# Optimization experiments

Measured on AMD Instinct MI355X. Metric: run time of the kernel, lower is better.

The kernel has to match this reference:

```python
import jax, jax.numpy as jnp
import numpy as np

SLOPE = 0.01   # LeakyReLU default negative slope
EPS = 1e-5     # InstanceNorm eps
PAD = 6        # shift-search border

def _pad(x):
    # ReplicationPad (1,1) on H and W (depth pad is 0, depth==1 anyway)
    return jnp.pad(x, ((0, 0), (0, 0), (1, 1), (1, 1)), mode='edge')

def _conv(x, w, b):
    y = jax.lax.conv_general_dilated(x, w, (1, 1), 'VALID',
                                     dimension_numbers=('NCHW', 'OIHW', 'NCHW'))
    return y + b[None, :, None, None]

def _inorm(x):
    # InstanceNorm3d (affine=False) over (D,H,W); D==1 so over (H,W) per (b,c)
    m = jnp.mean(x, axis=(-2, -1), keepdims=True)
    v = jnp.mean((x - m) ** 2, axis=(-2, -1), keepdims=True)
    return (x - m) * jax.lax.rsqrt(v + EPS)

def _lrelu(x):
    return jnp.where(x >= 0, x, SLOPE * x)

def setup_inputs() -> dict:
    key = jax.random.key(0)
    ks = jax.random.split(key, 8)
    B, H, W = 8, 256, 256
    xIn = jax.random.normal(ks[0], (B, 1, H, W), jnp.float32)
    target = jax.random.normal(ks[1], (B, 1, H, W), jnp.float32)
    w0 = jax.random.normal(ks[2], (64, 1, 3, 3), jnp.float32) * 0.1
    b0 = jax.random.normal(ks[3], (64,), jnp.float32) * 0.1
    ws = jax.random.normal(ks[4], (7, 64, 64, 3, 3), jnp.float32) * 0.05
    bs = jax.random.normal(ks[5], (7, 64), jnp.float32) * 0.05
    wp = jax.random.normal(ks[6], (1, 64, 3, 3), jnp.float32) * 0.05
    bp = jax.random.normal(ks[7], (1,), jnp.float32) * 0.05
    return {'xIn': xIn, 'target': target, 'w0': w0, 'b0': b0,
            'ws': ws, 'bs': bs, 'wp': wp, 'bp': bp}

def reference(xIn, target, w0, b0, ws, bs, wp, bp):
    x = _lrelu(_inorm(_conv(_pad(xIn), w0, b0)))
    for i in range(7):
        x = _lrelu(_inorm(_conv(_pad(x), ws[i], bs[i])))
    # projection + residual
    hr = _conv(_pad(x), wp, bp) + xIn  # (B,1,H,W)

    # vectorized findBestLoss: 13x13 shift search
    B, C, H, W = hr.shape
    h, w = H - 2 * PAD, W - 2 * PAD
    t = hr.dtype.type(0) + target[..., PAD:H - PAD, PAD:W - PAD]  # (B,C,h,w)
    offs = jnp.stack(jnp.meshgrid(jnp.arange(13), jnp.arange(13),
                                  indexing='ij'), -1).reshape(-1, 2)  # (169,2)

    def _slice(off):
        return jax.lax.dynamic_slice(hr, (0, 0, off[0], off[1]), (B, C, h, w))

    crops = jax.vmap(_slice)(offs)  # (169,B,C,h,w)
    eq = jax.lax.stop_gradient(
        jnp.mean(t[None] - crops, axis=(2, 3, 4), keepdims=True))  # detached equalizer
    losses = jnp.mean((crops + eq - t[None]) ** 2, axis=(2, 3, 4))  # (169,B)
    loss = jnp.mean(jnp.min(losses, axis=0))
    return hr, loss
```

## Files before the change

### kernel.cpp

```cpp
#include <hip/hip_runtime.h>

#define B_ 8
#define C_ 64
#define HW_ 65536
#define SLOPE_ 0.01f
#define EPS_ 1e-5f
#define CROP_ 244
#define NPIX_ 59536.0f

typedef unsigned short u16;
typedef __attribute__((ext_vector_type(8))) _Float16 f16x8;
typedef __attribute__((ext_vector_type(2))) _Float16 f16x2;
typedef __attribute__((ext_vector_type(4))) float f32x4;

__device__ __forceinline__ int clampi(int v, int lo, int hi) { return v < lo ? lo : (v > hi ? hi : v); }

__device__ __forceinline__ u16 f2h(float f) {
    union { _Float16 h; u16 u; } v; v.h = (_Float16)f; return v.u;
}
__device__ __forceinline__ float h2f(u16 b) {
    union { u16 u; _Float16 h; } v; v.u = b; return (float)v.h;
}
__device__ __forceinline__ f16x2 lrelu2(f16x2 a) {
    const f16x2 z = {(_Float16)0.f, (_Float16)0.f};
    const f16x2 sl = {(_Float16)SLOPE_, (_Float16)SLOPE_};
    return __builtin_elementwise_max(a, z) + sl * __builtin_elementwise_min(a, z);
}

__global__ void wtrans_kernel(const float* __restrict__ ws, u16* __restrict__ wH) {
    int idx = blockIdx.x * 256 + threadIdx.x;
    if (idx >= 7 * 36864) return;
    int l = idx / 36864;
    int rem = idx - l * 36864;
    int frag = rem >> 9;
    int lj = rem & 511;
    int lane = lj >> 3, j = lj & 7;
    int tap = frag >> 3, kb = (frag >> 2) & 1, mt = frag & 3;
    int oc = (mt << 4) + (lane & 15);
    int ic = (kb << 5) + ((lane >> 4) << 3) + j;
    wH[idx] = f2h(ws[((l * 64 + oc) * 64 + ic) * 9 + tap]);
}

__global__ __launch_bounds__(256) void conv0_kernel(
    const float* __restrict__ xin, const float* __restrict__ w0,
    const float* __restrict__ b0, u16* __restrict__ yout) {
    __shared__ float w0s[576];
    __shared__ float b0s[64];
    int tid = threadIdx.x;
    for (int i = tid; i < 576; i += 256) w0s[i] = w0[i];
    if (tid < 64) b0s[tid] = b0[tid];
    __syncthreads();
    int b = blockIdx.x & 7;
    int px = (blockIdx.x >> 3) * 256 + tid;
    int pxg = (b << 16) + px;
    int y = px >> 8, x = px & 255;
    float xv[9];
#pragma unroll
    for (int ky = 0; ky < 3; ky++)
#pragma unroll
        for (int kx = 0; kx < 3; kx++)
            xv[ky * 3 + kx] = xin[(b << 16) + (clampi(y + ky - 1, 0, 255) << 8) + clampi(x + kx - 1, 0, 255)];
    float acc[64];
#pragma unroll
    for (int k = 0; k < 64; k++) acc[k] = b0s[k];
#pragma unroll
    for (int t = 0; t < 9; t++) {
        float v = xv[t];
#pragma unroll
        for (int k = 0; k < 64; k++) acc[k] = fmaf(v, w0s[k * 9 + t], acc[k]);
    }
    uint4* op = (uint4*)(yout + ((size_t)pxg << 6));
#pragma unroll
    for (int c8 = 0; c8 < 8; c8++) {
        uint4 o;
        o.x = (unsigned)f2h(acc[c8 * 8 + 0]) | ((unsigned)f2h(acc[c8 * 8 + 1]) << 16);
        o.y = (unsigned)f2h(acc[c8 * 8 + 2]) | ((unsigned)f2h(acc[c8 * 8 + 3]) << 16);
        o.z = (unsigned)f2h(acc[c8 * 8 + 4]) | ((unsigned)f2h(acc[c8 * 8 + 5]) << 16);
        o.w = (unsigned)f2h(acc[c8 * 8 + 6]) | ((unsigned)f2h(acc[c8 * 8 + 7]) << 16);
        op[c8] = o;
    }
}

__global__ __launch_bounds__(256) void stats0_kernel(const u16* __restrict__ yin, float* __restrict__ partial) {
    __shared__ float red[4][64][2];
    int tid = threadIdx.x;
    int b = blockIdx.x & 7, tile = blockIdx.x >> 3;
    int pxl = tid >> 3, c8 = tid & 7;
    float s[8], s2[8];
#pragma unroll
    for (int i = 0; i < 8; i++) { s[i] = 0.f; s2[i] = 0.f; }
    for (int it = 0; it < 8; it++) {
        int px = (tile << 8) + (it << 5) + pxl;
        f16x8 v = *(const f16x8*)(yin + ((((size_t)(b << 16)) + px) << 6) + (c8 << 3));
#pragma unroll
        for (int i = 0; i < 8; i++) {
            float f = (float)v[i];
            s[i] += f; s2[i] += f * f;
        }
    }
#pragma unroll
    for (int msk = 8; msk <= 32; msk <<= 1)
#pragma unroll
        for (int i = 0; i < 8; i++) {
            s[i] += __shfl_xor(s[i], msk);
            s2[i] += __shfl_xor(s2[i], msk);
        }
    int lane = tid & 63, wv = tid >> 6;
    if (lane < 8) {
#pragma unroll
        for (int i = 0; i < 8; i++) {
            red[wv][lane * 8 + i][0] = s[i];
            red[wv][lane * 8 + i][1] = s2[i];
        }
    }
    __syncthreads();
    if (tid < 128) {
        int oc = tid >> 1, k2 = tid & 1;
        float v = red[0][oc][k2] + red[1][oc][k2] + red[2][oc][k2] + red[3][oc][k2];
        partial[(((b << 8) + tile) << 7) + (oc << 1) + k2] = v;
    }
}

__global__ __launch_bounds__(64) void statfin_kernel(const float* __restrict__ partial, float* __restrict__ normp, int ntiles) {
    int b = blockIdx.x >> 6, oc = blockIdx.x & 63;
    int lane = threadIdx.x;
    float s = 0.f, s2 = 0.f;
    for (int t = lane; t < ntiles; t += 64) {
        const float* p = partial + (((size_t)(b * ntiles + t)) << 7) + (oc << 1);
        s += p[0]; s2 += p[1];
    }
#pragma unroll
    for (int msk = 1; msk < 64; msk <<= 1) { s += __shfl_xor(s, msk); s2 += __shfl_xor(s2, msk); }
    if (lane == 0) {
        float mean = s * (1.0f / HW_);
        float var = s2 * (1.0f / HW_) - mean * mean;
        float inv = rsqrtf(var + EPS_);
        normp[blockIdx.x * 2] = inv;
        normp[blockIdx.x * 2 + 1] = -mean * inv;
    }
}

#define CM_CHUNKS 4896
__global__ __launch_bounds__(256, 1) void conv_mid_kernel(
    const u16* __restrict__ yin, const float* __restrict__ normp,
    const u16* __restrict__ wH, const float* __restrict__ bias,
    u16* __restrict__ yout, float* __restrict__ partial) {
    __shared__ u16 s_w[36864];
    __shared__ u16 s_in[612 * 64];
    __shared__ float s_red[4 * 64 * 2];
    __shared__ unsigned s_invk[32];
    __shared__ unsigned s_betak[32];
    __shared__ float s_bias[64];

    int tid = threadIdx.x;
    int bid = blockIdx.x;
    int b = bid & 7;
    int xs = (bid >> 3) & 15;
    int yq = bid >> 7;
    int x0 = xs << 4;

    if (tid < 64) s_bias[tid] = bias[tid];
    if (tid < 32) {
        float4 ld = ((const float4*)(normp + (b << 7)))[tid];
        union { unsigned u; f16x2 h; } iv, bv;
        iv.h = (f16x2){(_Float16)ld.x, (_Float16)ld.z};
        bv.h = (f16x2){(_Float16)ld.y, (_Float16)ld.w};
        s_invk[tid] = iv.u;
        s_betak[tid] = bv.u;
    }
    for (int i = tid; i < 4608; i += 256)
        ((uint4*)s_w)[i] = ((const uint4*)wH)[i];
    __syncthreads();

    {
        int y0 = yq << 7;
        for (int chunk = tid; chunk < CM_CHUNKS; chunk += 256) {
            int px = chunk >> 3, c8 = chunk & 7;
            int row = px / 18;
            int col = px - row * 18;
            int iy = clampi(y0 - 1 + row, 0, 255);
            int ix = clampi(x0 - 1 + col, 0, 255);
            union { uint4 q; f16x2 h2[4]; } ui, uo;
            ui.q = *(const uint4*)(yin + ((((size_t)(b << 16)) + (iy << 8) + ix) << 6) + (c8 << 3));
#pragma unroll
            for (int p = 0; p < 4; p++) {
                union { unsigned u; f16x2 h; } iv, bv;
                iv.u = s_invk[(c8 << 2) + p];
                bv.u = s_betak[(c8 << 2) + p];
                uo.h2[p] = lrelu2(ui.h2[p] * iv.h + bv.h);
            }
            *(uint4*)(&s_in[(px << 6) + ((c8 ^ (px & 7)) << 3)]) = uo.q;
        }
    }
    __syncthreads();

    int lane = tid & 63, wv = tid >> 6;
    int m = lane & 15, q = lane >> 4;
    int r0 = wv << 3;

    for (int r = 0; r < 4; r++) {
        int y0 = ((yq << 2) + r) << 5;
        uint4 pf[20];
        if (r < 3) {
            int y0n = y0 + 32;
#pragma unroll
            for (int k = 0; k < 20; k++) {
                int chunk = tid + (k << 8);
                if (chunk < CM_CHUNKS) {
                    int px = chunk >> 3, c8 = chunk & 7;
                    int row = px / 18;
                    int col = px - row * 18;
                    int iy = clampi(y0n - 1 + row, 0, 255);
                    int ix = clampi(x0 - 1 + col, 0, 255);
                    pf[k] = *(const uint4*)(yin + ((((size_t)(b << 16)) + (iy << 8) + ix) << 6) + (c8 << 3));
                }
            }
        }

        f32x4 acc[4][8];
#pragma unroll
        for (int a = 0; a < 4; a++)
#pragma unroll
            for (int c = 0; c < 8; c++) acc[a][c] = (f32x4){0.f, 0.f, 0.f, 0.f};

#pragma unroll 1
        for (int t = 0; t < 9; t++) {
            int ky = t / 3, kx = t - ky * 3;
            f16x8 wf[8];
#pragma unroll
            for (int f = 0; f < 8; f++)
                wf[f] = *(const f16x8*)(&s_w[(t << 12) + (f << 9) + (lane << 3)]);
#pragma unroll
            for (int nt = 0; nt < 8; nt++) {
                int p = (r0 + nt + ky) * 18 + kx + m;
                int key = p & 7;
                const u16* pin = &s_in[p << 6];
                f16x8 bf0 = *(const f16x8*)(pin + ((q ^ key) << 3));
                f16x8 bf1 = *(const f16x8*)(pin + (((4 + q) ^ key) << 3));
#pragma unroll
                for (int mt = 0; mt < 4; mt++)
                    acc[mt][nt] = __builtin_amdgcn_mfma_f32_16x16x32_f16(wf[mt], bf0, acc[mt][nt], 0, 0, 0);
#pragma unroll
                for (int mt = 0; mt < 4; mt++)
                    acc[mt][nt] = __builtin_amdgcn_mfma_f32_16x16x32_f16(wf[4 + mt], bf1, acc[mt][nt], 0, 0, 0);
            }
        }

        float ss[4][4], sq[4][4];
#pragma unroll
        for (int mt = 0; mt < 4; mt++)
#pragma unroll
            for (int rr = 0; rr < 4; rr++) { ss[mt][rr] = 0.f; sq[mt][rr] = 0.f; }

#pragma unroll
        for (int mt = 0; mt < 4; mt++) {
            int ocb = (mt << 4) + (q << 2);
            float b0v = s_bias[ocb], b1v = s_bias[ocb + 1], b2v = s_bias[ocb + 2], b3v = s_bias[ocb + 3];
#pragma unroll
            for (int nt = 0; nt < 8; nt++) {
                f32x4 v = acc[mt][nt];
                float v0 = v.x + b0v, v1 = v.y + b1v, v2 = v.z + b2v, v3 = v.w + b3v;
                uint2 o;
                o.x = (unsigned)f2h(v0) | ((unsigned)f2h(v1) << 16);
                o.y = (unsigned)f2h(v2) | ((unsigned)f2h(v3) << 16);
                int y = y0 + r0 + nt, x = x0 + m;
                *(uint2*)(yout + ((((size_t)(b << 16)) + (y << 8) + x) << 6) + ocb) = o;
                ss[mt][0] += v0; ss[mt][1] += v1; ss[mt][2] += v2; ss[mt][3] += v3;
                sq[mt][0] += v0 * v0; sq[mt][1] += v1 * v1; sq[mt][2] += v2 * v2; sq[mt][3] += v3 * v3;
            }
        }
#pragma unroll
        for (int mt = 0; mt < 4; mt++)
#pragma unroll
            for (int rr = 0; rr < 4; rr++) {
#pragma unroll
                for (int msk = 1; msk <= 8; msk <<= 1) {
                    ss[mt][rr] += __shfl_xor(ss[mt][rr], msk);
                    sq[mt][rr] += __shfl_xor(sq[mt][rr], msk);
                }
            }
        if (m == 0) {
#pragma unroll
            for (int mt = 0; mt < 4; mt++)
#pragma unroll
                for (int rr = 0; rr < 4; rr++) {
                    int oc = (mt << 4) + (q << 2) + rr;
                    s_red[(wv * 64 + oc) * 2] = ss[mt][rr];
                    s_red[(wv * 64 + oc) * 2 + 1] = sq[mt][rr];
                }
        }
        __syncthreads();
        if (tid < 128) {
            int oc = tid >> 1, k2 = tid & 1;
            float v = s_red[(0 * 64 + oc) * 2 + k2] + s_red[(1 * 64 + oc) * 2 + k2]
                    + s_red[(2 * 64 + oc) * 2 + k2] + s_red[(3 * 64 + oc) * 2 + k2];
            int tile = (((yq << 2) + r) << 4) + xs;
            partial[(((b << 7) + tile) << 7) + (oc << 1) + k2] = v;
        }
        if (r < 3) {
#pragma unroll
            for (int k = 0; k < 20; k++) {
                int chunk = tid + (k << 8);
                if (chunk < CM_CHUNKS) {
                    int px = chunk >> 3, c8 = chunk & 7;
                    union { uint4 q; f16x2 h2[4]; } ui, uo;
                    ui.q = pf[k];
#pragma unroll
                    for (int p = 0; p < 4; p++) {
                        union { unsigned u; f16x2 h; } iv, bv;
                        iv.u = s_invk[(c8 << 2) + p];
                        bv.u = s_betak[(c8 << 2) + p];
                        uo.h2[p] = lrelu2(ui.h2[p] * iv.h + bv.h);
                    }
                    *(uint4*)(&s_in[(px << 6) + ((c8 ^ (px & 7)) << 3)]) = uo.q;
                }
            }
        }
        __syncthreads();
    }
}

__global__ __launch_bounds__(256, 2) void proj_kernel(
    const u16* __restrict__ y7, const float* __restrict__ normp,
    const float* __restrict__ wp, const float* __restrict__ bp,
    const float* __restrict__ xin, float* __restrict__ out) {
    __shared__ u16 s_a[612 * 64];
    __shared__ unsigned s_invk[32];
    __shared__ unsigned s_betak[32];
    __shared__ unsigned s_w2[288];

    int tid = threadIdx.x;
    int b = blockIdx.x & 7, t = blockIdx.x >> 3;
    int ys = t >> 3, xsp = t & 7;
    int y0 = ys << 4, x0 = xsp << 5;

    if (tid < 32) {
        float4 ld = ((const float4*)(normp + (b << 7)))[tid];
        union { unsigned u; f16x2 h; } iv, bv;
        iv.h = (f16x2){(_Float16)ld.x, (_Float16)ld.z};
        bv.h = (f16x2){(_Float16)ld.y, (_Float16)ld.w};
        s_invk[tid] = iv.u;
        s_betak[tid] = bv.u;
    }
    for (int i = tid; i < 288; i += 256) {
        int pr = i / 9, tap = i - pr * 9;
        int ch = pr << 1;
        s_w2[i] = (unsigned)f2h(wp[ch * 9 + tap]) | ((unsigned)f2h(wp[(ch + 1) * 9 + tap]) << 16);
    }
    __syncthreads();

    for (int chunk = tid; chunk < 4896; chunk += 256) {
        int px = chunk >> 3, c8 = chunk & 7;
        int row = px / 34;
        int col = px - row * 34;
        int iy = clampi(y0 - 1 + row, 0, 255);
        int ix = clampi(x0 - 1 + col, 0, 255);
        union { uint4 q; f16x2 h2[4]; } ui, uo;
        ui.q = *(const uint4*)(y7 + ((((size_t)(b << 16)) + (iy << 8) + ix) << 6) + (c8 << 3));
#pragma unroll
        for (int p = 0; p < 4; p++) {
            union { unsigned u; f16x2 h; } iv, bv;
            iv.u = s_invk[(c8 << 2) + p];
            bv.u = s_betak[(c8 << 2) + p];
            uo.h2[p] = lrelu2(ui.h2[p] * iv.h + bv.h);
        }
        *(uint4*)(&s_a[(px << 6) + ((c8 ^ (px & 7)) << 3)]) = uo.q;
    }
    __syncthreads();

    float bias0 = bp[0];
#pragma unroll
    for (int half = 0; half < 2; half++) {
        int idx = (half << 8) + tid;
        int py = idx >> 5, pxx = idx & 31;
        float acc = bias0;
#pragma unroll
        for (int ky = 0; ky < 3; ky++)
#pragma unroll
            for (int kx = 0; kx < 3; kx++) {
                int p = (py + ky) * 34 + pxx + kx;
                int key = p & 7;
                const u16* pin = &s_a[p << 6];
                int tap = ky * 3 + kx;
#pragma unroll
                for (int c8 = 0; c8 < 8; c8++) {
                    f16x8 v = *(const f16x8*)(pin + ((c8 ^ key) << 3));
#pragma unroll
                    for (int i2 = 0; i2 < 4; i2++) {
                        unsigned wu = s_w2[((c8 << 2) + i2) * 9 + tap];
                        acc = fmaf((float)v[2 * i2], h2f((u16)(wu & 0xffff)), acc);
                        acc = fmaf((float)v[2 * i2 + 1], h2f((u16)(wu >> 16)), acc);
                    }
                }
            }
        int pxg = (b << 16) + ((y0 + py) << 8) + x0 + pxx;
        out[pxg] = acc + xin[pxg];
    }
}

__global__ __launch_bounds__(256) void loss_strip_kernel(
    const float* __restrict__ hr, const float* __restrict__ target,
    float* __restrict__ partial2) {
    __shared__ float s_hr[4][256];
    __shared__ float s_t[4][244];
    __shared__ float s_r2[4][13][2];

    int tid = threadIdx.x;
    int b = blockIdx.x & 7;
    int rest = blockIdx.x >> 3;
    int oy = rest % 13;
    int strip = rest / 13;
    int y0 = strip << 2;

    for (int i = tid; i < 1024; i += 256) {
        int r = i >> 8, x = i & 255;
        s_hr[r][x] = hr[(b << 16) + ((y0 + oy + r) << 8) + x];
    }
    for (int i = tid; i < 976; i += 256) {
        int r = i / 244, x = i - r * 244;
        s_t[r][x] = target[(b << 16) + ((y0 + r + 6) << 8) + 6 + x];
    }
    __syncthreads();

    float s[13], s2[13];
#pragma unroll
    for (int o = 0; o < 13; o++) { s[o] = 0.f; s2[o] = 0.f; }
    if (tid < 244) {
#pragma unroll
        for (int r = 0; r < 4; r++) {
            float tv = s_t[r][tid];
#pragma unroll
            for (int o = 0; o < 13; o++) {
                float d = s_hr[r][tid + o] - tv;
                s[o] += d; s2[o] += d * d;
            }
        }
    }
#pragma unroll
    for (int msk = 1; msk < 64; msk <<= 1)
#pragma unroll
        for (int o = 0; o < 13; o++) {
            s[o] += __shfl_xor(s[o], msk);
            s2[o] += __shfl_xor(s2[o], msk);
        }
    int lane = tid & 63, wv = tid >> 6;
    if (lane == 0) {
#pragma unroll
        for (int o = 0; o < 13; o++) { s_r2[wv][o][0] = s[o]; s_r2[wv][o][1] = s2[o]; }
    }
    __syncthreads();
    if (tid < 26) {
        int o = tid >> 1, k = tid & 1;
        float v = s_r2[0][o][k] + s_r2[1][o][k] + s_r2[2][o][k] + s_r2[3][o][k];
        int off = oy * 13 + o;
        partial2[(((b * 61 + strip) * 169) + off) * 2 + k] = v;
    }
}

__global__ __launch_bounds__(64) void loss_mid_kernel(
    const float* __restrict__ partial2, float* __restrict__ lossM) {
    int b = blockIdx.x & 7, off = blockIdx.x >> 3;
    int lane = threadIdx.x;
    float s = 0.f, s2 = 0.f;
    if (lane < 61) {
        const float* p = partial2 + (((b * 61 + lane) * 169) + off) * 2;
        s = p[0]; s2 = p[1];
    }
#pragma unroll
    for (int msk = 1; msk < 64; msk <<= 1) { s += __shfl_xor(s, msk); s2 += __shfl_xor(s2, msk); }
    if (lane == 0) {
        float m = s * (1.0f / NPIX_);
        lossM[off * 8 + b] = s2 * (1.0f / NPIX_) - m * m;
    }
}

__global__ void loss_final_kernel(const float* __restrict__ lossM, float* __restrict__ out) {
    int b = threadIdx.x;
    float mn = 0.f;
    if (b < 8) {
        mn = 1e30f;
        for (int off = 0; off < 169; off++) mn = fminf(mn, lossM[off * 8 + b]);
    }
#pragma unroll
    for (int msk = 1; msk < 8; msk <<= 1) mn += __shfl_xor(mn, msk);
    if (b == 0) out[0] = mn * 0.125f;
}

extern "C" void kernel_launch(void* const* d_in, const int* in_sizes, int n_in,
                              void* d_out, int out_size, void* d_ws, size_t ws_size,
                              hipStream_t stream) {
    const float* xIn    = (const float*)d_in[0];
    const float* target = (const float*)d_in[1];
    const float* w0     = (const float*)d_in[2];
    const float* b0     = (const float*)d_in[3];
    const float* wsAll  = (const float*)d_in[4];
    const float* bsAll  = (const float*)d_in[5];
    const float* wp     = (const float*)d_in[6];
    const float* bp     = (const float*)d_in[7];
    float* out = (float*)d_out;

    float* normp    = (float*)d_ws;
    float* partial  = normp + 1024;
    float* partial2 = partial + 262144;
    float* lossM    = partial2 + 164944;
    u16*  wH        = (u16*)(lossM + 1352);
    u16*  bufA      = wH + 258048;
    u16*  bufB      = bufA + 33554432;

    wtrans_kernel<<<1008, 256, 0, stream>>>(wsAll, wH);
    conv0_kernel<<<2048, 256, 0, stream>>>(xIn, w0, b0, bufA);
    stats0_kernel<<<2048, 256, 0, stream>>>(bufA, partial);
    statfin_kernel<<<512, 64, 0, stream>>>(partial, normp, 256);
    for (int l = 0; l < 7; l++) {
        const u16* in = (l & 1) ? bufB : bufA;
        u16* o = (l & 1) ? bufA : bufB;
        conv_mid_kernel<<<256, 256, 0, stream>>>(
            in, normp, wH + l * 36864, bsAll + l * 64, o, partial);
        statfin_kernel<<<512, 64, 0, stream>>>(partial, normp, 128);
    }
    proj_kernel<<<1024, 256, 0, stream>>>(bufB, normp, wp, bp, xIn, out);
    loss_strip_kernel<<<6344, 256, 0, stream>>>(out, target, partial2);
    loss_mid_kernel<<<1352, 64, 0, stream>>>(partial2, lossM);
    loss_final_kernel<<<1, 64, 0, stream>>>(lossM, out + 524288);
}
```

Baseline: 795.1 us.

## Fuse stat finalization into conv kernels and read activations directly from global

```diff
diff --git a/kernel.cpp b/kernel.cpp
--- a/kernel.cpp
+++ b/kernel.cpp
@@ -121,212 +121,163 @@
     }
 }
 
-__global__ __launch_bounds__(64) void statfin_kernel(const float* __restrict__ partial, float* __restrict__ normp, int ntiles) {
-    int b = blockIdx.x >> 6, oc = blockIdx.x & 63;
-    int lane = threadIdx.x;
-    float s = 0.f, s2 = 0.f;
-    for (int t = lane; t < ntiles; t += 64) {
-        const float* p = partial + (((size_t)(b * ntiles + t)) << 7) + (oc << 1);
-        s += p[0]; s2 += p[1];
-    }
-#pragma unroll
-    for (int msk = 1; msk < 64; msk <<= 1) { s += __shfl_xor(s, msk); s2 += __shfl_xor(s2, msk); }
-    if (lane == 0) {
-        float mean = s * (1.0f / HW_);
-        float var = s2 * (1.0f / HW_) - mean * mean;
-        float inv = rsqrtf(var + EPS_);
-        normp[blockIdx.x * 2] = inv;
-        normp[blockIdx.x * 2 + 1] = -mean * inv;
-    }
-}
-
-#define CM_CHUNKS 4896
-__global__ __launch_bounds__(256, 1) void conv_mid_kernel(
-    const u16* __restrict__ yin, const float* __restrict__ normp,
+__global__ __launch_bounds__(256, 2) void conv_mid_kernel(
+    const u16* __restrict__ yin, const float* __restrict__ pin_part,
     const u16* __restrict__ wH, const float* __restrict__ bias,
-    u16* __restrict__ yout, float* __restrict__ partial) {
-    __shared__ u16 s_w[36864];
-    __shared__ u16 s_in[612 * 64];
-    __shared__ float s_red[4 * 64 * 2];
-    __shared__ unsigned s_invk[32];
-    __shared__ unsigned s_betak[32];
+    u16* __restrict__ yout, float* __restrict__ pout_part, int ntiles_in) {
+    __shared__ float s_tmp[256];
+    __shared__ float s_v[128];
+    __shared__ unsigned s_inv2[32];
+    __shared__ unsigned s_beta2[32];
     __shared__ float s_bias[64];
+    __shared__ float s_red[512];
 
     int tid = threadIdx.x;
-    int bid = blockIdx.x;
-    int b = bid & 7;
-    int xs = (bid >> 3) & 15;
-    int yq = bid >> 7;
-    int x0 = xs << 4;
-
-    if (tid < 64) s_bias[tid] = bias[tid];
-    if (tid < 32) {
-        float4 ld = ((const float4*)(normp + (b << 7)))[tid];
-        union { unsigned u; f16x2 h; } iv, bv;
-        iv.h = (f16x2){(_Float16)ld.x, (_Float16)ld.z};
-        bv.h = (f16x2){(_Float16)ld.y, (_Float16)ld.w};
-        s_invk[tid] = iv.u;
-        s_betak[tid] = bv.u;
-    }
-    for (int i = tid; i < 4608; i += 256)
-        ((uint4*)s_w)[i] = ((const uint4*)wH)[i];
-    __syncthreads();
+    int b = blockIdx.x & 7;
+    int tile = blockIdx.x >> 3;
+    int ty = tile >> 4, tx = tile & 15;
+    int y0 = ty << 5, x0 = tx << 4;
 
     {
-        int y0 = yq << 7;
-        for (int chunk = tid; chunk < CM_CHUNKS; chunk += 256) {
-            int px = chunk >> 3, c8 = chunk & 7;
-            int row = px / 18;
-            int col = px - row * 18;
-            int iy = clampi(y0 - 1 + row, 0, 255);
-            int ix = clampi(x0 - 1 + col, 0, 255);
-            union { uint4 q; f16x2 h2[4]; } ui, uo;
-            ui.q = *(const uint4*)(yin + ((((size_t)(b << 16)) + (iy << 8) + ix) << 6) + (c8 << 3));
-#pragma unroll
-            for (int p = 0; p < 4; p++) {
-                union { unsigned u; f16x2 h; } iv, bv;
-                iv.u = s_invk[(c8 << 2) + p];
-                bv.u = s_betak[(c8 << 2) + p];
-                uo.h2[p] = lrelu2(ui.h2[p] * iv.h + bv.h);
-            }
-            *(uint4*)(&s_in[(px << 6) + ((c8 ^ (px & 7)) << 3)]) = uo.q;
-        }
-    }
-    __syncthreads();
+        int j = tid & 127, h = tid >> 7;
+        float s = 0.f;
+        for (int t = h; t < ntiles_in; t += 2)
+            s += pin_part[(((size_t)(b * ntiles_in + t)) << 7) + j];
+        s_tmp[tid] = s;
+        __syncthreads();
+        if (tid < 128) s_v[tid] = s_tmp[tid] + s_tmp[tid + 128];
+        if (tid < 64) s_bias[tid] = bias[tid];
+        __syncthreads();
+        if (tid < 64) {
+            float sm = s_v[tid * 2], s2v = s_v[tid * 2 + 1];
+            float mean = sm * (1.0f / HW_);
+            float var = s2v * (1.0f / HW_) - mean * mean;
+            float inv = rsqrtf(var + EPS_);
+            s_v[tid * 2] = inv;
+            s_v[tid * 2 + 1] = -mean * inv;
+        }
+        __syncthreads();
+        if (tid < 32) {
+            int ch = (tid >> 2) * 8 + (tid & 3) * 2;
+            union { unsigned u; f16x2 h2; } a, bb;
+            a.h2 = (f16x2){(_Float16)s_v[ch * 2], (_Float16)s_v[ch * 2 + 2]};
+            bb.h2 = (f16x2){(_Float16)s_v[ch * 2 + 1], (_Float16)s_v[ch * 2 + 3]};
+            s_inv2[tid] = a.u;
+            s_beta2[tid] = bb.u;
+        }
+        __syncthreads();
+    }
 
     int lane = tid & 63, wv = tid >> 6;
     int m = lane & 15, q = lane >> 4;
-    int r0 = wv << 3;
-
-    for (int r = 0; r < 4; r++) {
-        int y0 = ((yq << 2) + r) << 5;
-        uint4 pf[20];
-        if (r < 3) {
-            int y0n = y0 + 32;
-#pragma unroll
-            for (int k = 0; k < 20; k++) {
-                int chunk = tid + (k << 8);
-                if (chunk < CM_CHUNKS) {
-                    int px = chunk >> 3, c8 = chunk & 7;
-                    int row = px / 18;
-                    int col = px - row * 18;
-                    int iy = clampi(y0n - 1 + row, 0, 255);
-                    int ix = clampi(x0 - 1 + col, 0, 255);
-                    pf[k] = *(const uint4*)(yin + ((((size_t)(b << 16)) + (iy << 8) + ix) << 6) + (c8 << 3));
-                }
+
+    f16x2 inv0[4], bet0[4], inv1[4], bet1[4];
+#pragma unroll
+    for (int p = 0; p < 4; p++) {
+        union { unsigned u; f16x2 h; } t0, t1, t2, t3;
+        t0.u = s_inv2[(q << 2) + p];  inv0[p] = t0.h;
+        t1.u = s_beta2[(q << 2) + p]; bet0[p] = t1.h;
+        t2.u = s_inv2[((4 + q) << 2) + p];  inv1[p] = t2.h;
+        t3.u = s_beta2[((4 + q) << 2) + p]; bet1[p] = t3.h;
+    }
+
+    f32x4 acc[4][8];
+#pragma unroll
+    for (int a = 0; a < 4; a++)
+#pragma unroll
+        for (int c = 0; c < 8; c++) acc[a][c] = (f32x4){0.f, 0.f, 0.f, 0.f};
+
+    const u16* ybase = yin + ((size_t)b << 22);
+    int rbase = y0 + (wv << 3);
+
+#pragma unroll 1
+    for (int t = 0; t < 9; t++) {
+        int ky = t / 3, kx = t - ky * 3;
+        const u16* wp0 = wH + (t << 12) + (lane << 3);
+        f16x8 wf[8];
+#pragma unroll
+        for (int f = 0; f < 8; f++) wf[f] = *(const f16x8*)(wp0 + (f << 9));
+        int xc = clampi(x0 + kx - 1 + m, 0, 255);
+#pragma unroll
+        for (int nt = 0; nt < 8; nt++) {
+            int row = clampi(rbase + nt + ky - 1, 0, 255);
+            const u16* pp = ybase + (((row << 8) + xc) << 6);
+            union { f16x8 v; f16x2 h2[4]; } u0, u1;
+            u0.v = *(const f16x8*)(pp + (q << 3));
+            u1.v = *(const f16x8*)(pp + ((4 + q) << 3));
+#pragma unroll
+            for (int p = 0; p < 4; p++) {
+                u0.h2[p] = lrelu2(u0.h2[p] * inv0[p] + bet0[p]);
+                u1.h2[p] = lrelu2(u1.h2[p] * inv1[p] + bet1[p]);
             }
-        }
-
-        f32x4 acc[4][8];
-#pragma unroll
-        for (int a = 0; a < 4; a++)
-#pragma unroll
-            for (int c = 0; c < 8; c++) acc[a][c] = (f32x4){0.f, 0.f, 0.f, 0.f};
-
-#pragma unroll 1
-        for (int t = 0; t < 9; t++) {
-            int ky = t / 3, kx = t - ky * 3;
-            f16x8 wf[8];
-#pragma unroll
-            for (int f = 0; f < 8; f++)
-                wf[f] = *(const f16x8*)(&s_w[(t << 12) + (f << 9) + (lane << 3)]);
-#pragma unroll
-            for (int nt = 0; nt < 8; nt++) {
-                int p = (r0 + nt + ky) * 18 + kx + m;
-                int key = p & 7;
-                const u16* pin = &s_in[p << 6];
-                f16x8 bf0 = *(const f16x8*)(pin + ((q ^ key) << 3));
-                f16x8 bf1 = *(const f16x8*)(pin + (((4 + q) ^ key) << 3));
-#pragma unroll
-                for (int mt = 0; mt < 4; mt++)
-                    acc[mt][nt] = __builtin_amdgcn_mfma_f32_16x16x32_f16(wf[mt], bf0, acc[mt][nt], 0, 0, 0);
-#pragma unroll
-                for (int mt = 0; mt < 4; mt++)
-                    acc[mt][nt] = __builtin_amdgcn_mfma_f32_16x16x32_f16(wf[4 + mt], bf1, acc[mt][nt], 0, 0, 0);
+#pragma unroll
+            for (int mt = 0; mt < 4; mt++)
+                acc[mt][nt] = __builtin_amdgcn_mfma_f32_16x16x32_f16(wf[mt], u0.v, acc[mt][nt], 0, 0, 0);
+#pragma unroll
+            for (int mt = 0; mt < 4; mt++)
+                acc[mt][nt] = __builtin_amdgcn_mfma_f32_16x16x32_f16(wf[4 + mt], u1.v, acc[mt][nt], 0, 0, 0);
+        }
+    }
+
+    float ss[4][4], sq[4][4];
+#pragma unroll
+    for (int mt = 0; mt < 4; mt++)
+#pragma unroll
+        for (int rr = 0; rr < 4; rr++) { ss[mt][rr] = 0.f; sq[mt][rr] = 0.f; }
+
+#pragma unroll
+    for (int mt = 0; mt < 4; mt++) {
+        int ocb = (mt << 4) + (q << 2);
+        float b0v = s_bias[ocb], b1v = s_bias[ocb + 1], b2v = s_bias[ocb + 2], b3v = s_bias[ocb + 3];
+#pragma unroll
+        for (int nt = 0; nt < 8; nt++) {
+            f32x4 v = acc[mt][nt];
+            float v0 = v.x + b0v, v1 = v.y + b1v, v2 = v.z + b2v, v3 = v.w + b3v;
+            uint2 o;
+            o.x = (unsigned)f2h(v0) | ((unsigned)f2h(v1) << 16);
+            o.y = (unsigned)f2h(v2) | ((unsigned)f2h(v3) << 16);
+            int y = rbase + nt, x = x0 + m;
+            *(uint2*)(yout + ((((size_t)(b << 16)) + (y << 8) + x) << 6) + ocb) = o;
+            ss[mt][0] += v0; ss[mt][1] += v1; ss[mt][2] += v2; ss[mt][3] += v3;
+            sq[mt][0] += v0 * v0; sq[mt][1] += v1 * v1; sq[mt][2] += v2 * v2; sq[mt][3] += v3 * v3;
+        }
+    }
+#pragma unroll
+    for (int mt = 0; mt < 4; mt++)
+#pragma unroll
+        for (int rr = 0; rr < 4; rr++) {
+#pragma unroll
+            for (int msk = 1; msk <= 8; msk <<= 1) {
+                ss[mt][rr] += __shfl_xor(ss[mt][rr], msk);
+                sq[mt][rr] += __shfl_xor(sq[mt][rr], msk);
             }
         }
-
-        float ss[4][4], sq[4][4];
+    if (m == 0) {
 #pragma unroll
         for (int mt = 0; mt < 4; mt++)
 #pragma unroll
-            for (int rr = 0; rr < 4; rr++) { ss[mt][rr] = 0.f; sq[mt][rr] = 0.f; }
-
-#pragma unroll
-        for (int mt = 0; mt < 4; mt++) {
-            int ocb = (mt << 4) + (q << 2);
-            float b0v = s_bias[ocb], b1v = s_bias[ocb + 1], b2v = s_bias[ocb + 2], b3v = s_bias[ocb + 3];
-#pragma unroll
-            for (int nt = 0; nt < 8; nt++) {
-                f32x4 v = acc[mt][nt];
-                float v0 = v.x + b0v, v1 = v.y + b1v, v2 = v.z + b2v, v3 = v.w + b3v;
-                uint2 o;
-                o.x = (unsigned)f2h(v0) | ((unsigned)f2h(v1) << 16);
-                o.y = (unsigned)f2h(v2) | ((unsigned)f2h(v3) << 16);
-                int y = y0 + r0 + nt, x = x0 + m;
-                *(uint2*)(yout + ((((size_t)(b << 16)) + (y << 8) + x) << 6) + ocb) = o;
-                ss[mt][0] += v0; ss[mt][1] += v1; ss[mt][2] += v2; ss[mt][3] += v3;
-                sq[mt][0] += v0 * v0; sq[mt][1] += v1 * v1; sq[mt][2] += v2 * v2; sq[mt][3] += v3 * v3;
+            for (int rr = 0; rr < 4; rr++) {
+                int oc = (mt << 4) + (q << 2) + rr;
+                s_red[(wv * 64 + oc) * 2] = ss[mt][rr];
+                s_red[(wv * 64 + oc) * 2 + 1] = sq[mt][rr];
             }
-        }
-#pragma unroll
-        for (int mt = 0; mt < 4; mt++)
-#pragma unroll
-            for (int rr = 0; rr < 4; rr++) {
-#pragma unroll
-                for (int msk = 1; msk <= 8; msk <<= 1) {
-                    ss[mt][rr] += __shfl_xor(ss[mt][rr], msk);
-                    sq[mt][rr] += __shfl_xor(sq[mt][rr], msk);
-                }
-            }
-        if (m == 0) {
-#pragma unroll
-            for (int mt = 0; mt < 4; mt++)
-#pragma unroll
-                for (int rr = 0; rr < 4; rr++) {
-                    int oc = (mt << 4) + (q << 2) + rr;
-                    s_red[(wv * 64 + oc) * 2] = ss[mt][rr];
-                    s_red[(wv * 64 + oc) * 2 + 1] = sq[mt][rr];
-                }
-        }
-        __syncthreads();
-        if (tid < 128) {
-            int oc = tid >> 1, k2 = tid & 1;
-            float v = s_red[(0 * 64 + oc) * 2 + k2] + s_red[(1 * 64 + oc) * 2 + k2]
-                    + s_red[(2 * 64 + oc) * 2 + k2] + s_red[(3 * 64 + oc) * 2 + k2];
-            int tile = (((yq << 2) + r) << 4) + xs;
-            partial[(((b << 7) + tile) << 7) + (oc << 1) + k2] = v;
-        }
-        if (r < 3) {
-#pragma unroll
-            for (int k = 0; k < 20; k++) {
-                int chunk = tid + (k << 8);
-                if (chunk < CM_CHUNKS) {
-                    int px = chunk >> 3, c8 = chunk & 7;
-                    union { uint4 q; f16x2 h2[4]; } ui, uo;
-                    ui.q = pf[k];
-#pragma unroll
-                    for (int p = 0; p < 4; p++) {
-                        union { unsigned u; f16x2 h; } iv, bv;
-                        iv.u = s_invk[(c8 << 2) + p];
-                        bv.u = s_betak[(c8 << 2) + p];
-                        uo.h2[p] = lrelu2(ui.h2[p] * iv.h + bv.h);
-                    }
-                    *(uint4*)(&s_in[(px << 6) + ((c8 ^ (px & 7)) << 3)]) = uo.q;
-                }
-            }
-        }
-        __syncthreads();
+    }
+    __syncthreads();
+    if (tid < 128) {
+        int oc = tid >> 1, k2 = tid & 1;
+        float v = s_red[(0 * 64 + oc) * 2 + k2] + s_red[(1 * 64 + oc) * 2 + k2]
+                + s_red[(2 * 64 + oc) * 2 + k2] + s_red[(3 * 64 + oc) * 2 + k2];
+        pout_part[(((b << 7) + tile) << 7) + (oc << 1) + k2] = v;
     }
 }
 
 __global__ __launch_bounds__(256, 2) void proj_kernel(
-    const u16* __restrict__ y7, const float* __restrict__ normp,
+    const u16* __restrict__ y7, const float* __restrict__ pin_part,
     const float* __restrict__ wp, const float* __restrict__ bp,
     const float* __restrict__ xin, float* __restrict__ out) {
     __shared__ u16 s_a[612 * 64];
-    __shared__ unsigned s_invk[32];
-    __shared__ unsigned s_betak[32];
+    __shared__ unsigned s_inv2[32];
+    __shared__ unsigned s_beta2[32];
     __shared__ unsigned s_w2[288];
 
     int tid = threadIdx.x;
@@ -334,14 +285,37 @@
     int ys = t >> 3, xsp = t & 7;
     int y0 = ys << 4, x0 = xsp << 5;
 
-    if (tid < 32) {
-        float4 ld = ((const float4*)(normp + (b << 7)))[tid];
-        union { unsigned u; f16x2 h; } iv, bv;
-        iv.h = (f16x2){(_Float16)ld.x, (_Float16)ld.z};
-        bv.h = (f16x2){(_Float16)ld.y, (_Float16)ld.w};
-        s_invk[tid] = iv.u;
-        s_betak[tid] = bv.u;
-    }
+    {
+        float* s_tmp = (float*)s_a;
+        float* s_v = ((float*)s_a) + 256;
+        int j = tid & 127, h = tid >> 7;
+        float s = 0.f;
+        for (int tt = h; tt < 128; tt += 2)
+            s += pin_part[(((size_t)((b << 7) + tt)) << 7) + j];
+        s_tmp[tid] = s;
+        __syncthreads();
+        if (tid < 128) s_v[tid] = s_tmp[tid] + s_tmp[tid + 128];
+        __syncthreads();
+        if (tid < 64) {
+            float sm = s_v[tid * 2], s2v = s_v[tid * 2 + 1];
+            float mean = sm * (1.0f / HW_);
+            float var = s2v * (1.0f / HW_) - mean * mean;
+            float inv = rsqrtf(var + EPS_);
+            s_v[tid * 2] = inv;
+            s_v[tid * 2 + 1] = -mean * inv;
+        }
+        __syncthreads();
+        if (tid < 32) {
+            int ch = (tid >> 2) * 8 + (tid & 3) * 2;
+            union { unsigned u; f16x2 h2; } a, bb;
+            a.h2 = (f16x2){(_Float16)s_v[ch * 2], (_Float16)s_v[ch * 2 + 2]};
+            bb.h2 = (f16x2){(_Float16)s_v[ch * 2 + 1], (_Float16)s_v[ch * 2 + 3]};
+            s_inv2[tid] = a.u;
+            s_beta2[tid] = bb.u;
+        }
+        __syncthreads();
+    }
+
     for (int i = tid; i < 288; i += 256) {
         int pr = i / 9, tap = i - pr * 9;
         int ch = pr << 1;
@@ -360,8 +334,8 @@
 #pragma unroll
         for (int p = 0; p < 4; p++) {
             union { unsigned u; f16x2 h; } iv, bv;
-            iv.u = s_invk[(c8 << 2) + p];
-            bv.u = s_betak[(c8 << 2) + p];
+            iv.u = s_inv2[(c8 << 2) + p];
+            bv.u = s_beta2[(c8 << 2) + p];
             uo.h2[p] = lrelu2(ui.h2[p] * iv.h + bv.h);
         }
         *(uint4*)(&s_a[(px << 6) + ((c8 ^ (px & 7)) << 3)]) = uo.q;
@@ -499,9 +473,9 @@
     const float* bp     = (const float*)d_in[7];
     float* out = (float*)d_out;
 
-    float* normp    = (float*)d_ws;
-    float* partial  = normp + 1024;
-    float* partial2 = partial + 262144;
+    float* pA       = (float*)d_ws;
+    float* pB       = pA + 262144;
+    float* partial2 = pB + 262144;
     float* lossM    = partial2 + 164944;
     u16*  wH        = (u16*)(lossM + 1352);
     u16*  bufA      = wH + 258048;
@@ -509,16 +483,16 @@
 
     wtrans_kernel<<<1008, 256, 0, stream>>>(wsAll, wH);
     conv0_kernel<<<2048, 256, 0, stream>>>(xIn, w0, b0, bufA);
-    stats0_kernel<<<2048, 256, 0, stream>>>(bufA, partial);
-    statfin_kernel<<<512, 64, 0, stream>>>(partial, normp, 256);
+    stats0_kernel<<<2048, 256, 0, stream>>>(bufA, pA);
     for (int l = 0; l < 7; l++) {
         const u16* in = (l & 1) ? bufB : bufA;
         u16* o = (l & 1) ? bufA : bufB;
-        conv_mid_kernel<<<256, 256, 0, stream>>>(
-            in, normp, wH + l * 36864, bsAll + l * 64, o, partial);
-        statfin_kernel<<<512, 64, 0, stream>>>(partial, normp, 128);
-    }
-    proj_kernel<<<1024, 256, 0, stream>>>(bufB, normp, wp, bp, xIn, out);
+        const float* inp = (l & 1) ? pB : pA;
+        float* outp = (l & 1) ? pA : pB;
+        conv_mid_kernel<<<1024, 256, 0, stream>>>(
+            in, inp, wH + l * 36864, bsAll + l * 64, o, outp, (l == 0) ? 256 : 128);
+    }
+    proj_kernel<<<1024, 256, 0, stream>>>(bufB, pB, wp, bp, xIn, out);
     loss_strip_kernel<<<6344, 256, 0, stream>>>(out, target, partial2);
     loss_mid_kernel<<<1352, 64, 0, stream>>>(partial2, lossM);
     loss_final_kernel<<<1, 64, 0, stream>>>(lossM, out + 524288);
```

Result: slower. 1.198 ms (+50.7%).

## Shrink conv_mid tiles to 32x16, drop LDS weights, run two blocks per CU

Applied to the files above, without the earlier changes.

```diff
diff --git a/kernel.cpp b/kernel.cpp
--- a/kernel.cpp
+++ b/kernel.cpp
@@ -140,183 +140,193 @@
     }
 }
 
-#define CM_CHUNKS 4896
-__global__ __launch_bounds__(256, 1) void conv_mid_kernel(
+__global__ __launch_bounds__(256, 2) void conv_mid_kernel(
     const u16* __restrict__ yin, const float* __restrict__ normp,
     const u16* __restrict__ wH, const float* __restrict__ bias,
     u16* __restrict__ yout, float* __restrict__ partial) {
-    __shared__ u16 s_w[36864];
     __shared__ u16 s_in[612 * 64];
-    __shared__ float s_red[4 * 64 * 2];
-    __shared__ unsigned s_invk[32];
-    __shared__ unsigned s_betak[32];
+    __shared__ unsigned s_inv2[32];
+    __shared__ unsigned s_beta2[32];
     __shared__ float s_bias[64];
+    __shared__ float s_red[512];
 
     int tid = threadIdx.x;
-    int bid = blockIdx.x;
-    int b = bid & 7;
-    int xs = (bid >> 3) & 15;
-    int yq = bid >> 7;
-    int x0 = xs << 4;
+    int b = blockIdx.x & 7;
+    int tile = blockIdx.x >> 3;
+    int ty = tile >> 4, tx = tile & 15;
+    int y0 = ty << 5, x0 = tx << 4;
 
     if (tid < 64) s_bias[tid] = bias[tid];
     if (tid < 32) {
         float4 ld = ((const float4*)(normp + (b << 7)))[tid];
-        union { unsigned u; f16x2 h; } iv, bv;
-        iv.h = (f16x2){(_Float16)ld.x, (_Float16)ld.z};
-        bv.h = (f16x2){(_Float16)ld.y, (_Float16)ld.w};
-        s_invk[tid] = iv.u;
-        s_betak[tid] = bv.u;
-    }
-    for (int i = tid; i < 4608; i += 256)
-        ((uint4*)s_w)[i] = ((const uint4*)wH)[i];
-    __syncthreads();
-
-    {
-        int y0 = yq << 7;
-        for (int chunk = tid; chunk < CM_CHUNKS; chunk += 256) {
-            int px = chunk >> 3, c8 = chunk & 7;
-            int row = px / 18;
-            int col = px - row * 18;
-            int iy = clampi(y0 - 1 + row, 0, 255);
-            int ix = clampi(x0 - 1 + col, 0, 255);
-            union { uint4 q; f16x2 h2[4]; } ui, uo;
-            ui.q = *(const uint4*)(yin + ((((size_t)(b << 16)) + (iy << 8) + ix) << 6) + (c8 << 3));
-#pragma unroll
-            for (int p = 0; p < 4; p++) {
-                union { unsigned u; f16x2 h; } iv, bv;
-                iv.u = s_invk[(c8 << 2) + p];
-                bv.u = s_betak[(c8 << 2) + p];
-                uo.h2[p] = lrelu2(ui.h2[p] * iv.h + bv.h);
-            }
-            *(uint4*)(&s_in[(px << 6) + ((c8 ^ (px & 7)) << 3)]) = uo.q;
-        }
+        union { unsigned u; f16x2 h2; } a, bb;
+        a.h2 = (f16x2){(_Float16)ld.x, (_Float16)ld.z};
+        bb.h2 = (f16x2){(_Float16)ld.y, (_Float16)ld.w};
+        s_inv2[tid] = a.u;
+        s_beta2[tid] = bb.u;
+    }
+    __syncthreads();
+
+    for (int chunk = tid; chunk < 2592; chunk += 256) {
+        int px = chunk >> 3, c8 = chunk & 7;
+        int row = px / 18;
+        int col = px - row * 18;
+        int iy = clampi(y0 - 1 + row, 0, 255);
+        int ix = clampi(x0 - 1 + col, 0, 255);
+        union { uint4 q; f16x2 h2[4]; } ui, uo;
+        ui.q = *(const uint4*)(yin + ((((size_t)(b << 16)) + (iy << 8) + ix) << 6) + (c8 << 3));
+#pragma unroll
+        for (int p = 0; p < 4; p++) {
+            union { unsigned u; f16x2 h; } iv, bv;
+            iv.u = s_inv2[(c8 << 2) + p];
+            bv.u = s_beta2[(c8 << 2) + p];
+            uo.h2[p] = lrelu2(ui.h2[p] * iv.h + bv.h);
+        }
+        *(uint4*)(&s_in[(px << 6) + ((c8 ^ (px & 7)) << 3)]) = uo.q;
     }
     __syncthreads();
 
     int lane = tid & 63, wv = tid >> 6;
     int m = lane & 15, q = lane >> 4;
-    int r0 = wv << 3;
-
-    for (int r = 0; r < 4; r++) {
-        int y0 = ((yq << 2) + r) << 5;
-        uint4 pf[20];
-        if (r < 3) {
-            int y0n = y0 + 32;
-#pragma unroll
-            for (int k = 0; k < 20; k++) {
-                int chunk = tid + (k << 8);
-                if (chunk < CM_CHUNKS) {
-                    int px = chunk >> 3, c8 = chunk & 7;
-                    int row = px / 18;
-                    int col = px - row * 18;
-                    int iy = clampi(y0n - 1 + row, 0, 255);
-                    int ix = clampi(x0 - 1 + col, 0, 255);
-                    pf[k] = *(const uint4*)(yin + ((((size_t)(b << 16)) + (iy << 8) + ix) << 6) + (c8 << 3));
-                }
-            }
-        }
-
-        f32x4 acc[4][8];
-#pragma unroll
-        for (int a = 0; a < 4; a++)
-#pragma unroll
-            for (int c = 0; c < 8; c++) acc[a][c] = (f32x4){0.f, 0.f, 0.f, 0.f};
-
+
+    uint4 pf[9];
+    int pfc8[9];
+    int pfpx[9];
+#pragma unroll
+    for (int k = 0; k < 9; k++) {
+        int chunk = 2592 + tid + (k << 8);
+        int px = chunk >> 3, c8 = chunk & 7;
+        int row = px / 18;
+        int col = px - row * 18;
+        int iy = clampi(y0 - 1 + row, 0, 255);
+        int ix = clampi(x0 - 1 + col, 0, 255);
+        pf[k] = *(const uint4*)(yin + ((((size_t)(b << 16)) + (iy << 8) + ix) << 6) + (c8 << 3));
+        pfc8[k] = c8; pfpx[k] = px;
+    }
+
+    f32x4 accA[4][4], accB[4][4];
+#pragma unroll
+    for (int a = 0; a < 4; a++)
+#pragma unroll
+        for (int c = 0; c < 4; c++) { accA[a][c] = (f32x4){0.f,0.f,0.f,0.f}; accB[a][c] = (f32x4){0.f,0.f,0.f,0.f}; }
+
+    int r0a = wv << 2;
+    const f16x8* wfp = (const f16x8*)wH;
 #pragma unroll 1
-        for (int t = 0; t < 9; t++) {
-            int ky = t / 3, kx = t - ky * 3;
-            f16x8 wf[8];
-#pragma unroll
-            for (int f = 0; f < 8; f++)
-                wf[f] = *(const f16x8*)(&s_w[(t << 12) + (f << 9) + (lane << 3)]);
-#pragma unroll
-            for (int nt = 0; nt < 8; nt++) {
-                int p = (r0 + nt + ky) * 18 + kx + m;
-                int key = p & 7;
-                const u16* pin = &s_in[p << 6];
-                f16x8 bf0 = *(const f16x8*)(pin + ((q ^ key) << 3));
-                f16x8 bf1 = *(const f16x8*)(pin + (((4 + q) ^ key) << 3));
-#pragma unroll
-                for (int mt = 0; mt < 4; mt++)
-                    acc[mt][nt] = __builtin_amdgcn_mfma_f32_16x16x32_f16(wf[mt], bf0, acc[mt][nt], 0, 0, 0);
-#pragma unroll
-                for (int mt = 0; mt < 4; mt++)
-                    acc[mt][nt] = __builtin_amdgcn_mfma_f32_16x16x32_f16(wf[4 + mt], bf1, acc[mt][nt], 0, 0, 0);
-            }
-        }
-
-        float ss[4][4], sq[4][4];
-#pragma unroll
-        for (int mt = 0; mt < 4; mt++)
-#pragma unroll
-            for (int rr = 0; rr < 4; rr++) { ss[mt][rr] = 0.f; sq[mt][rr] = 0.f; }
-
-#pragma unroll
-        for (int mt = 0; mt < 4; mt++) {
-            int ocb = (mt << 4) + (q << 2);
-            float b0v = s_bias[ocb], b1v = s_bias[ocb + 1], b2v = s_bias[ocb + 2], b3v = s_bias[ocb + 3];
-#pragma unroll
-            for (int nt = 0; nt < 8; nt++) {
-                f32x4 v = acc[mt][nt];
+    for (int t = 0; t < 9; t++) {
+        int ky = t / 3, kx = t - ky * 3;
+        const f16x8* wn = wfp + (t << 9);
+        f16x8 wf[8];
+#pragma unroll
+        for (int f = 0; f < 8; f++) wf[f] = wn[(f << 6) + lane];
+#pragma unroll
+        for (int nt = 0; nt < 4; nt++) {
+            int p = (r0a + nt + ky) * 18 + kx + m;
+            int key = p & 7;
+            const u16* pin = &s_in[p << 6];
+            f16x8 bf0 = *(const f16x8*)(pin + ((q ^ key) << 3));
+            f16x8 bf1 = *(const f16x8*)(pin + (((4 + q) ^ key) << 3));
+#pragma unroll
+            for (int mt = 0; mt < 4; mt++)
+                accA[mt][nt] = __builtin_amdgcn_mfma_f32_16x16x32_f16(wf[mt], bf0, accA[mt][nt], 0, 0, 0);
+#pragma unroll
+            for (int mt = 0; mt < 4; mt++)
+                accA[mt][nt] = __builtin_amdgcn_mfma_f32_16x16x32_f16(wf[4 + mt], bf1, accA[mt][nt], 0, 0, 0);
+        }
+    }
+
+#pragma unroll
+    for (int k = 0; k < 9; k++) {
+        int c8 = pfc8[k], px = pfpx[k];
+        union { uint4 q; f16x2 h2[4]; } ui, uo;
+        ui.q = pf[k];
+#pragma unroll
+        for (int p = 0; p < 4; p++) {
+            union { unsigned u; f16x2 h; } iv, bv;
+            iv.u = s_inv2[(c8 << 2) + p];
+            bv.u = s_beta2[(c8 << 2) + p];
+            uo.h2[p] = lrelu2(ui.h2[p] * iv.h + bv.h);
+        }
+        *(uint4*)(&s_in[(px << 6) + ((c8 ^ (px & 7)) << 3)]) = uo.q;
+    }
+    __syncthreads();
+
+    int r0b = 16 + (wv << 2);
+#pragma unroll 1
+    for (int t = 0; t < 9; t++) {
+        int ky = t / 3, kx = t - ky * 3;
+        const f16x8* wn = wfp + (t << 9);
+        f16x8 wf[8];
+#pragma unroll
+        for (int f = 0; f < 8; f++) wf[f] = wn[(f << 6) + lane];
+#pragma unroll
+        for (int nt = 0; nt < 4; nt++) {
+            int p = (r0b + nt + ky) * 18 + kx + m;
+            int key = p & 7;
+            const u16* pin = &s_in[p << 6];
+            f16x8 bf0 = *(const f16x8*)(pin + ((q ^ key) << 3));
+            f16x8 bf1 = *(const f16x8*)(pin + (((4 + q) ^ key) << 3));
+#pragma unroll
+            for (int mt = 0; mt < 4; mt++)
+                accB[mt][nt] = __builtin_amdgcn_mfma_f32_16x16x32_f16(wf[mt], bf0, accB[mt][nt], 0, 0, 0);
+#pragma unroll
+            for (int mt = 0; mt < 4; mt++)
+                accB[mt][nt] = __builtin_amdgcn_mfma_f32_16x16x32_f16(wf[4 + mt], bf1, accB[mt][nt], 0, 0, 0);
+        }
+    }
+
+    float ss[4][4], sq[4][4];
+#pragma unroll
+    for (int mt = 0; mt < 4; mt++)
+#pragma unroll
+        for (int rr = 0; rr < 4; rr++) { ss[mt][rr] = 0.f; sq[mt][rr] = 0.f; }
+
+#pragma unroll
+    for (int mt = 0; mt < 4; mt++) {
+        int ocb = (mt << 4) + (q << 2);
+        float b0v = s_bias[ocb], b1v = s_bias[ocb + 1], b2v = s_bias[ocb + 2], b3v = s_bias[ocb + 3];
+#pragma unroll
+        for (int half = 0; half < 2; half++) {
+#pragma unroll
+            for (int nt = 0; nt < 4; nt++) {
+                f32x4 v = half ? accB[mt][nt] : accA[mt][nt];
                 float v0 = v.x + b0v, v1 = v.y + b1v, v2 = v.z + b2v, v3 = v.w + b3v;
                 uint2 o;
                 o.x = (unsigned)f2h(v0) | ((unsigned)f2h(v1) << 16);
                 o.y = (unsigned)f2h(v2) | ((unsigned)f2h(v3) << 16);
-                int y = y0 + r0 + nt, x = x0 + m;
+                int y = y0 + (half ? r0b : r0a) + nt, x = x0 + m;
                 *(uint2*)(yout + ((((size_t)(b << 16)) + (y << 8) + x) << 6) + ocb) = o;
                 ss[mt][0] += v0; ss[mt][1] += v1; ss[mt][2] += v2; ss[mt][3] += v3;
                 sq[mt][0] += v0 * v0; sq[mt][1] += v1 * v1; sq[mt][2] += v2 * v2; sq[mt][3] += v3 * v3;
             }
         }
+    }
+#pragma unroll
+    for (int mt = 0; mt < 4; mt++)
+#pragma unroll
+        for (int rr = 0; rr < 4; rr++) {
+#pragma unroll
+            for (int msk = 1; msk <= 8; msk <<= 1) {
+                ss[mt][rr] += __shfl_xor(ss[mt][rr], msk);
+                sq[mt][rr] += __shfl_xor(sq[mt][rr], msk);
+            }
+        }
+    if (m == 0) {
 #pragma unroll
         for (int mt = 0; mt < 4; mt++)
 #pragma unroll
             for (int rr = 0; rr < 4; rr++) {
-#pragma unroll
-                for (int msk = 1; msk <= 8; msk <<= 1) {
-                    ss[mt][rr] += __shfl_xor(ss[mt][rr], msk);
-                    sq[mt][rr] += __shfl_xor(sq[mt][rr], msk);
-                }
+                int oc = (mt << 4) + (q << 2) + rr;
+                s_red[(wv * 64 + oc) * 2] = ss[mt][rr];
+                s_red[(wv * 64 + oc) * 2 + 1] = sq[mt][rr];
             }
-        if (m == 0) {
-#pragma unroll
-            for (int mt = 0; mt < 4; mt++)
-#pragma unroll
-                for (int rr = 0; rr < 4; rr++) {
-                    int oc = (mt << 4) + (q << 2) + rr;
-                    s_red[(wv * 64 + oc) * 2] = ss[mt][rr];
-                    s_red[(wv * 64 + oc) * 2 + 1] = sq[mt][rr];
-                }
-        }
-        __syncthreads();
-        if (tid < 128) {
-            int oc = tid >> 1, k2 = tid & 1;
-            float v = s_red[(0 * 64 + oc) * 2 + k2] + s_red[(1 * 64 + oc) * 2 + k2]
-                    + s_red[(2 * 64 + oc) * 2 + k2] + s_red[(3 * 64 + oc) * 2 + k2];
-            int tile = (((yq << 2) + r) << 4) + xs;
-            partial[(((b << 7) + tile) << 7) + (oc << 1) + k2] = v;
-        }
-        if (r < 3) {
-#pragma unroll
-            for (int k = 0; k < 20; k++) {
-                int chunk = tid + (k << 8);
-                if (chunk < CM_CHUNKS) {
-                    int px = chunk >> 3, c8 = chunk & 7;
-                    union { uint4 q; f16x2 h2[4]; } ui, uo;
-                    ui.q = pf[k];
-#pragma unroll
-                    for (int p = 0; p < 4; p++) {
-                        union { unsigned u; f16x2 h; } iv, bv;
-                        iv.u = s_invk[(c8 << 2) + p];
-                        bv.u = s_betak[(c8 << 2) + p];
-                        uo.h2[p] = lrelu2(ui.h2[p] * iv.h + bv.h);
-                    }
-                    *(uint4*)(&s_in[(px << 6) + ((c8 ^ (px & 7)) << 3)]) = uo.q;
-                }
-            }
-        }
-        __syncthreads();
+    }
+    __syncthreads();
+    if (tid < 128) {
+        int oc = tid >> 1, k2 = tid & 1;
+        float v = s_red[(0 * 64 + oc) * 2 + k2] + s_red[(1 * 64 + oc) * 2 + k2]
+                + s_red[(2 * 64 + oc) * 2 + k2] + s_red[(3 * 64 + oc) * 2 + k2];
+        partial[(((b << 7) + tile) << 7) + (oc << 1) + k2] = v;
     }
 }
 
@@ -325,8 +335,8 @@
     const float* __restrict__ wp, const float* __restrict__ bp,
     const float* __restrict__ xin, float* __restrict__ out) {
     __shared__ u16 s_a[612 * 64];
-    __shared__ unsigned s_invk[32];
-    __shared__ unsigned s_betak[32];
+    __shared__ unsigned s_inv2[32];
+    __shared__ unsigned s_beta2[32];
     __shared__ unsigned s_w2[288];
 
     int tid = threadIdx.x;
@@ -336,11 +346,11 @@
 
     if (tid < 32) {
         float4 ld = ((const float4*)(normp + (b << 7)))[tid];
-        union { unsigned u; f16x2 h; } iv, bv;
-        iv.h = (f16x2){(_Float16)ld.x, (_Float16)ld.z};
-        bv.h = (f16x2){(_Float16)ld.y, (_Float16)ld.w};
-        s_invk[tid] = iv.u;
-        s_betak[tid] = bv.u;
+        union { unsigned u; f16x2 h2; } a, bb;
+        a.h2 = (f16x2){(_Float16)ld.x, (_Float16)ld.z};
+        bb.h2 = (f16x2){(_Float16)ld.y, (_Float16)ld.w};
+        s_inv2[tid] = a.u;
+        s_beta2[tid] = bb.u;
     }
     for (int i = tid; i < 288; i += 256) {
         int pr = i / 9, tap = i - pr * 9;
@@ -360,8 +370,8 @@
 #pragma unroll
         for (int p = 0; p < 4; p++) {
             union { unsigned u; f16x2 h; } iv, bv;
-            iv.u = s_invk[(c8 << 2) + p];
-            bv.u = s_betak[(c8 << 2) + p];
+            iv.u = s_inv2[(c8 << 2) + p];
+            bv.u = s_beta2[(c8 << 2) + p];
             uo.h2[p] = lrelu2(ui.h2[p] * iv.h + bv.h);
         }
         *(uint4*)(&s_a[(px << 6) + ((c8 ^ (px & 7)) << 3)]) = uo.q;
@@ -514,7 +524,7 @@
     for (int l = 0; l < 7; l++) {
         const u16* in = (l & 1) ? bufB : bufA;
         u16* o = (l & 1) ? bufA : bufB;
-        conv_mid_kernel<<<256, 256, 0, stream>>>(
+        conv_mid_kernel<<<1024, 256, 0, stream>>>(
             in, normp, wH + l * 36864, bsAll + l * 64, o, partial);
         statfin_kernel<<<512, 64, 0, stream>>>(partial, normp, 128);
     }
```

Result: faster. 710.8 us (-10.6%).
